# Performance work log

Measured on AMD Instinct MI355X. Metric: run time of the kernel, lower is better.

## Reference

```python
import jax, jax.numpy as jnp
import numpy as np

NUM_USERS = 100000
NUM_ITEMS = 100000
SEQ_LEN = 32
EMBED_DIM = 64
FC_DIM = 100
BATCH = 512
T = 3  # number of target items per example (train mode)


def setup_inputs() -> dict:
    key = jax.random.key(0)
    ks = jax.random.split(key, 12)
    seq_var = jax.random.randint(ks[0], (BATCH, SEQ_LEN), 0, NUM_ITEMS)
    user_var = jax.random.randint(ks[1], (BATCH, 1), 0, NUM_USERS)
    item_var = jax.random.randint(ks[2], (BATCH, T), 0, NUM_ITEMS)
    # Embedding tables, init normal(0, 1/dim) as in the torch module
    item_emb = jax.random.normal(ks[3], (NUM_ITEMS, EMBED_DIM)) * (1.0 / EMBED_DIM)
    user_emb = jax.random.normal(ks[4], (NUM_USERS, EMBED_DIM)) * (1.0 / EMBED_DIM)
    W2 = jax.random.normal(ks[5], (NUM_ITEMS, FC_DIM + EMBED_DIM)) * (1.0 / (FC_DIM + EMBED_DIM))
    b2 = jnp.zeros((NUM_ITEMS, 1))
    # nn.Linear default init: U(-1/sqrt(fan_in), 1/sqrt(fan_in))
    lim1 = 1.0 / np.sqrt(2 * EMBED_DIM)
    W1 = jax.random.uniform(ks[6], (FC_DIM, 2 * EMBED_DIM), minval=-lim1, maxval=lim1)
    b1 = jax.random.uniform(ks[7], (FC_DIM,), minval=-lim1, maxval=lim1)
    lim2 = 1.0 / np.sqrt(FC_DIM)
    Wf2 = jax.random.uniform(ks[8], (FC_DIM, FC_DIM), minval=-lim2, maxval=lim2)
    bf2 = jax.random.uniform(ks[9], (FC_DIM,), minval=-lim2, maxval=lim2)
    return dict(seq_var=seq_var, user_var=user_var, item_var=item_var,
                item_emb=item_emb, user_emb=user_emb, W2=W2, b2=b2,
                W1=W1, b1=b1, Wf2=Wf2, bf2=bf2)


def reference(seq_var, user_var, item_var, item_emb, user_emb, W2, b2, W1, b1, Wf2, bf2):
    # Dropout is identity in eval mode.
    d = item_emb.shape[1]
    embs = item_emb[seq_var]          # [B, L, d]
    uemb = user_emb[user_var]         # [B, 1, d]
    # fc1 on concat(item_i, item_j): split W1 columns so we never build the
    # [B, L, L, 2d] concat tensor; same math as Linear(cat([i, j])).
    Wa, Wb = W1[:, :d], W1[:, d:]     # [FC, d] each
    # all_embed[b, a, c] = cat(embs[b, c], embs[b, a])  (item_i varies with c)
    A = jnp.einsum('bld,fd->blf', embs, Wa)   # applied to item_i (index c)
    Bm = jnp.einsum('bld,fd->blf', embs, Wb)  # applied to item_j (index a)
    h = jax.nn.relu(A[:, None, :, :] + Bm[:, :, None, :] + b1)  # [B, L, L, FC]
    h = jax.nn.relu(jnp.einsum('bacf,gf->bacg', h, Wf2) + bf2)  # [B, L, L, FC]
    x = h.sum((1, 2))                               # [B, FC]
    x = jnp.concatenate([x, uemb[:, 0, :]], axis=1)  # [B, FC + d]
    w2 = W2[item_var]                                # [B, T, FC+d]
    bb = b2[item_var]                                # [B, T, 1]
    out = bb[..., 0] + jnp.einsum('btf,bf->bt', w2, x)  # baddbmm + squeeze -> [B, T]
    return out
```

## Files before the change

kernel.cpp:

```cpp
#include <hip/hip_runtime.h>

typedef float f32x4 __attribute__((ext_vector_type(4)));
typedef short short8 __attribute__((ext_vector_type(8)));
typedef _Float16 half8 __attribute__((ext_vector_type(8)));

#define SEQ_LEN 32
#define EMBED_DIM 64
#define FC_DIM 100
#define BATCH 512
#define AS 136
#define ES 72

union Frag {
  half8 h8;
  _Float16 h[8];
  short8 s;
  unsigned int u[4];
};

__global__ __launch_bounds__(256, 2) void cosrec_fused(
    const int* __restrict__ seq_var, const int* __restrict__ user_var,
    const int* __restrict__ item_var, const float* __restrict__ item_emb,
    const float* __restrict__ user_emb, const float* __restrict__ W2,
    const float* __restrict__ b2, const float* __restrict__ W1,
    const float* __restrict__ b1, const float* __restrict__ Wf2,
    const float* __restrict__ bf2, float* __restrict__ out)
{
  __shared__ __align__(16) _Float16 A_s[SEQ_LEN * AS];
  __shared__ __align__(16) _Float16 B_s[SEQ_LEN * AS];
  __shared__ float red_s[16 * 112];
  __shared__ float x_s[112];
  __shared__ __align__(16) _Float16 emb_s[SEQ_LEN * ES];

  const int b = blockIdx.x;
  const int t = threadIdx.x;
  const int w = t >> 6;
  const int l = t & 63;
  const int l15 = l & 15;
  const int q = l >> 4;
  const unsigned int biasbits = (q == 0) ? 0x00003C00u : 0u;

  {
    const int r = t >> 3;
    const int c0 = (t & 7) * 8;
    const int item = seq_var[b * SEQ_LEN + r];
    const float4 v0 = *(const float4*)(item_emb + item * EMBED_DIM + c0);
    const float4 v1 = *(const float4*)(item_emb + item * EMBED_DIM + c0 + 4);
    Frag e;
    e.h[0] = (_Float16)v0.x; e.h[1] = (_Float16)v0.y;
    e.h[2] = (_Float16)v0.z; e.h[3] = (_Float16)v0.w;
    e.h[4] = (_Float16)v1.x; e.h[5] = (_Float16)v1.y;
    e.h[6] = (_Float16)v1.z; e.h[7] = (_Float16)v1.w;
    *(short8*)(emb_s + r * ES + c0) = e.s;
  }
  for (int i = t; i < SEQ_LEN * 14; i += 256) {
    const int r = i / 14, d = (i % 14) * 2;
    *(unsigned int*)(A_s + r * AS + FC_DIM + d) = 0u;
    *(unsigned int*)(B_s + r * AS + FC_DIM + d) = 0u;
  }

  Frag wfrag[7][4];
  #pragma unroll
  for (int nt = 0; nt < 7; ++nt) {
    const int gg = nt * 16 + l15;
    const bool gok = (gg < FC_DIM);
    #pragma unroll
    for (int ks = 0; ks < 3; ++ks) {
      Frag f;
      if (gok) {
        const float4 u0 = *(const float4*)(Wf2 + gg * FC_DIM + ks * 32 + q * 8);
        const float4 u1 = *(const float4*)(Wf2 + gg * FC_DIM + ks * 32 + q * 8 + 4);
        f.h[0] = (_Float16)u0.x; f.h[1] = (_Float16)u0.y;
        f.h[2] = (_Float16)u0.z; f.h[3] = (_Float16)u0.w;
        f.h[4] = (_Float16)u1.x; f.h[5] = (_Float16)u1.y;
        f.h[6] = (_Float16)u1.z; f.h[7] = (_Float16)u1.w;
      } else {
        f.u[0] = 0u; f.u[1] = 0u; f.u[2] = 0u; f.u[3] = 0u;
      }
      wfrag[nt][ks] = f;
    }
    Frag f3;
    f3.u[0] = 0u; f3.u[1] = 0u; f3.u[2] = 0u; f3.u[3] = 0u;
    if (gok && q == 0) {
      const float4 u0 = *(const float4*)(Wf2 + gg * FC_DIM + 96);
      f3.h[0] = (_Float16)u0.x; f3.h[1] = (_Float16)u0.y;
      f3.h[2] = (_Float16)u0.z; f3.h[3] = (_Float16)u0.w;
      f3.h[4] = (_Float16)bf2[gg];
    }
    wfrag[nt][3] = f3;
  }
  __syncthreads();

  for (int nt = w; nt < 13; nt += 4) {
    const int o = nt * 16 + l15;
    int wr = 0, wc = 0;
    bool valid = true;
    if (o < FC_DIM)            { wr = o;          wc = 0;  }
    else if (o < 2 * FC_DIM)   { wr = o - FC_DIM; wc = 64; }
    else valid = false;
    Frag bfr[2];
    #pragma unroll
    for (int ks = 0; ks < 2; ++ks) {
      if (valid) {
        const float* p = W1 + wr * 128 + wc + ks * 32 + q * 8;
        const float4 u0 = *(const float4*)p;
        const float4 u1 = *(const float4*)(p + 4);
        bfr[ks].h[0] = (_Float16)u0.x; bfr[ks].h[1] = (_Float16)u0.y;
        bfr[ks].h[2] = (_Float16)u0.z; bfr[ks].h[3] = (_Float16)u0.w;
        bfr[ks].h[4] = (_Float16)u1.x; bfr[ks].h[5] = (_Float16)u1.y;
        bfr[ks].h[6] = (_Float16)u1.z; bfr[ks].h[7] = (_Float16)u1.w;
      } else {
        bfr[ks].u[0] = 0u; bfr[ks].u[1] = 0u; bfr[ks].u[2] = 0u; bfr[ks].u[3] = 0u;
      }
    }
    const float b1v = (o >= FC_DIM && o < 2 * FC_DIM) ? b1[o - FC_DIM] : 0.f;
    #pragma unroll
    for (int mt = 0; mt < 2; ++mt) {
      Frag afr[2];
      #pragma unroll
      for (int ks = 0; ks < 2; ++ks)
        afr[ks].s = *(const short8*)(emb_s + (mt * 16 + l15) * ES + ks * 32 + q * 8);
      f32x4 acc = {0.f, 0.f, 0.f, 0.f};
      #pragma unroll
      for (int ks = 0; ks < 2; ++ks)
        acc = __builtin_amdgcn_mfma_f32_16x16x32_f16(afr[ks].h8, bfr[ks].h8, acc, 0, 0, 0);
      const int row = mt * 16 + q * 4;
      if (o < FC_DIM) {
        #pragma unroll
        for (int r = 0; r < 4; ++r)
          A_s[(row + r) * AS + o] = (_Float16)acc[r];
      } else if (o < 2 * FC_DIM) {
        #pragma unroll
        for (int r = 0; r < 4; ++r)
          B_s[(row + r) * AS + (o - FC_DIM)] = (_Float16)(acc[r] + b1v);
      }
    }
  }
  __syncthreads();

  float colsum[7];
  #pragma unroll
  for (int nt = 0; nt < 7; ++nt) colsum[nt] = 0.f;
  const half8 hzero = {};

  for (int g = w; g < 8; g += 4) {
    const int c = (g & 1) * 16 + l15;
    const int a0 = (g >> 1) * 8;
    Frag areg[4];
    #pragma unroll
    for (int ks = 0; ks < 4; ++ks)
      areg[ks].s = *(const short8*)(A_s + c * AS + ks * 32 + q * 8);
    for (int ai = 0; ai < 8; ++ai) {
      const _Float16* bp = B_s + (a0 + ai) * AS;
      Frag hf[4];
      #pragma unroll
      for (int ks = 0; ks < 4; ++ks) {
        Frag br;
        br.s = *(const short8*)(bp + ks * 32 + q * 8);
        const half8 sum = areg[ks].h8 + br.h8;
        hf[ks].h8 = __builtin_elementwise_max(sum, hzero);
      }
      hf[3].u[2] |= biasbits;
      #pragma unroll
      for (int nt = 0; nt < 7; ++nt) {
        f32x4 acc = {0.f, 0.f, 0.f, 0.f};
        #pragma unroll
        for (int ks = 0; ks < 4; ++ks)
          acc = __builtin_amdgcn_mfma_f32_16x16x32_f16(hf[ks].h8, wfrag[nt][ks].h8, acc, 0, 0, 0);
        #pragma unroll
        for (int r = 0; r < 4; ++r)
          colsum[nt] += fmaxf(acc[r], 0.f);
      }
    }
  }

  #pragma unroll
  for (int nt = 0; nt < 7; ++nt)
    red_s[(w * 4 + q) * 112 + nt * 16 + l15] = colsum[nt];
  __syncthreads();
  if (t < 112) {
    float s = 0.f;
    #pragma unroll
    for (int r = 0; r < 16; ++r) s += red_s[r * 112 + t];
    x_s[t] = s;
  }
  __syncthreads();

  if (w < 3) {
    const int iv = item_var[b * 3 + w];
    const int uu = user_var[b];
    float partial = 0.f;
    for (int idx = l; idx < FC_DIM + EMBED_DIM; idx += 64) {
      const float xv = (idx < FC_DIM)
                           ? x_s[idx]
                           : user_emb[uu * EMBED_DIM + (idx - FC_DIM)];
      partial += W2[iv * (FC_DIM + EMBED_DIM) + idx] * xv;
    }
    #pragma unroll
    for (int off = 32; off > 0; off >>= 1)
      partial += __shfl_down(partial, off, 64);
    if (l == 0) out[b * 3 + w] = partial + b2[iv];
  }
}

extern "C" void kernel_launch(void* const* d_in, const int* in_sizes, int n_in,
                              void* d_out, int out_size, void* d_ws, size_t ws_size,
                              hipStream_t stream) {
  const int* seq = (const int*)d_in[0];
  const int* usr = (const int*)d_in[1];
  const int* itm = (const int*)d_in[2];
  const float* item_emb = (const float*)d_in[3];
  const float* user_emb = (const float*)d_in[4];
  const float* W2  = (const float*)d_in[5];
  const float* b2  = (const float*)d_in[6];
  const float* W1  = (const float*)d_in[7];
  const float* b1  = (const float*)d_in[8];
  const float* Wf2 = (const float*)d_in[9];
  const float* bf2 = (const float*)d_in[10];
  cosrec_fused<<<BATCH, 256, 0, stream>>>(seq, usr, itm, item_emb, user_emb,
                                          W2, b2, W1, b1, Wf2, bf2,
                                          (float*)d_out);
}
```

Measured before the change: 157.1 us.

## Prefetch W2/user/W1 operands early, double-buffer B rows, shuffle-based colsum reduction

Issues the W2 row, user embedding and b2 loads at kernel start so their latency overlaps the rest of the kernel. All W1 fragments are loaded into registers before the first barrier rather than inside the fc1 loop. In the pairwise loop, the next B_s row is prefetched into registers while the current row is computed. The column-sum reduction now uses wave shuffles followed by a single LDS pass, which removes one barrier and shrinks the reduction buffer, at the cost of higher register pressure.

```diff
diff --git a/kernel.cpp b/kernel.cpp
--- a/kernel.cpp
+++ b/kernel.cpp
@@ -28,8 +28,7 @@
 {
   __shared__ __align__(16) _Float16 A_s[SEQ_LEN * AS];
   __shared__ __align__(16) _Float16 B_s[SEQ_LEN * AS];
-  __shared__ float red_s[16 * 112];
-  __shared__ float x_s[112];
+  __shared__ float red_s[4 * 112];
   __shared__ __align__(16) _Float16 emb_s[SEQ_LEN * ES];
 
   const int b = blockIdx.x;
@@ -53,10 +52,17 @@
     e.h[6] = (_Float16)v1.z; e.h[7] = (_Float16)v1.w;
     *(short8*)(emb_s + r * ES + c0) = e.s;
   }
-  for (int i = t; i < SEQ_LEN * 14; i += 256) {
-    const int r = i / 14, d = (i % 14) * 2;
-    *(unsigned int*)(A_s + r * AS + FC_DIM + d) = 0u;
-    *(unsigned int*)(B_s + r * AS + FC_DIM + d) = 0u;
+
+  float w2a = 0.f, w2b = 0.f, w2c = 0.f, uev = 0.f, b2v = 0.f;
+  if (w < 3) {
+    const int iv = item_var[b * 3 + w];
+    const int uu = user_var[b];
+    const float* w2p = W2 + iv * (FC_DIM + EMBED_DIM);
+    w2a = w2p[l];
+    w2b = w2p[64 + l];
+    if (l < 36) w2c = w2p[128 + l];
+    uev = user_emb[uu * EMBED_DIM + (l >= 36 ? l - 36 : l + 28)];
+    b2v = b2[iv];
   }
 
   Frag wfrag[7][4];
@@ -89,50 +95,67 @@
     }
     wfrag[nt][3] = f3;
   }
+
+  Frag bfrh[4][2];
+  float b1h[4];
+  #pragma unroll
+  for (int i = 0; i < 4; ++i) {
+    const int nt = w + i * 4;
+    b1h[i] = 0.f;
+    bfrh[i][0].u[0] = 0u; bfrh[i][0].u[1] = 0u; bfrh[i][0].u[2] = 0u; bfrh[i][0].u[3] = 0u;
+    bfrh[i][1].u[0] = 0u; bfrh[i][1].u[1] = 0u; bfrh[i][1].u[2] = 0u; bfrh[i][1].u[3] = 0u;
+    if (nt < 13) {
+      const int o = nt * 16 + l15;
+      if (o < 2 * FC_DIM) {
+        const int wr = (o < FC_DIM) ? o : o - FC_DIM;
+        const int wc = (o < FC_DIM) ? 0 : 64;
+        #pragma unroll
+        for (int ks = 0; ks < 2; ++ks) {
+          const float* p = W1 + wr * 128 + wc + ks * 32 + q * 8;
+          const float4 u0 = *(const float4*)p;
+          const float4 u1 = *(const float4*)(p + 4);
+          bfrh[i][ks].h[0] = (_Float16)u0.x; bfrh[i][ks].h[1] = (_Float16)u0.y;
+          bfrh[i][ks].h[2] = (_Float16)u0.z; bfrh[i][ks].h[3] = (_Float16)u0.w;
+          bfrh[i][ks].h[4] = (_Float16)u1.x; bfrh[i][ks].h[5] = (_Float16)u1.y;
+          bfrh[i][ks].h[6] = (_Float16)u1.z; bfrh[i][ks].h[7] = (_Float16)u1.w;
+        }
+        if (o >= FC_DIM) b1h[i] = b1[o - FC_DIM];
+      }
+    }
+  }
+
+  for (int i = t; i < SEQ_LEN * 14; i += 256) {
+    const int r = i / 14, d = (i % 14) * 2;
+    *(unsigned int*)(A_s + r * AS + FC_DIM + d) = 0u;
+    *(unsigned int*)(B_s + r * AS + FC_DIM + d) = 0u;
+  }
   __syncthreads();
 
-  for (int nt = w; nt < 13; nt += 4) {
-    const int o = nt * 16 + l15;
-    int wr = 0, wc = 0;
-    bool valid = true;
-    if (o < FC_DIM)            { wr = o;          wc = 0;  }
-    else if (o < 2 * FC_DIM)   { wr = o - FC_DIM; wc = 64; }
-    else valid = false;
-    Frag bfr[2];
-    #pragma unroll
-    for (int ks = 0; ks < 2; ++ks) {
-      if (valid) {
-        const float* p = W1 + wr * 128 + wc + ks * 32 + q * 8;
-        const float4 u0 = *(const float4*)p;
-        const float4 u1 = *(const float4*)(p + 4);
-        bfr[ks].h[0] = (_Float16)u0.x; bfr[ks].h[1] = (_Float16)u0.y;
-        bfr[ks].h[2] = (_Float16)u0.z; bfr[ks].h[3] = (_Float16)u0.w;
-        bfr[ks].h[4] = (_Float16)u1.x; bfr[ks].h[5] = (_Float16)u1.y;
-        bfr[ks].h[6] = (_Float16)u1.z; bfr[ks].h[7] = (_Float16)u1.w;
-      } else {
-        bfr[ks].u[0] = 0u; bfr[ks].u[1] = 0u; bfr[ks].u[2] = 0u; bfr[ks].u[3] = 0u;
-      }
-    }
-    const float b1v = (o >= FC_DIM && o < 2 * FC_DIM) ? b1[o - FC_DIM] : 0.f;
-    #pragma unroll
-    for (int mt = 0; mt < 2; ++mt) {
-      Frag afr[2];
-      #pragma unroll
-      for (int ks = 0; ks < 2; ++ks)
-        afr[ks].s = *(const short8*)(emb_s + (mt * 16 + l15) * ES + ks * 32 + q * 8);
-      f32x4 acc = {0.f, 0.f, 0.f, 0.f};
-      #pragma unroll
-      for (int ks = 0; ks < 2; ++ks)
-        acc = __builtin_amdgcn_mfma_f32_16x16x32_f16(afr[ks].h8, bfr[ks].h8, acc, 0, 0, 0);
-      const int row = mt * 16 + q * 4;
-      if (o < FC_DIM) {
-        #pragma unroll
-        for (int r = 0; r < 4; ++r)
-          A_s[(row + r) * AS + o] = (_Float16)acc[r];
-      } else if (o < 2 * FC_DIM) {
-        #pragma unroll
-        for (int r = 0; r < 4; ++r)
-          B_s[(row + r) * AS + (o - FC_DIM)] = (_Float16)(acc[r] + b1v);
+  #pragma unroll
+  for (int i = 0; i < 4; ++i) {
+    const int nt = w + i * 4;
+    if (nt < 13) {
+      const int o = nt * 16 + l15;
+      #pragma unroll
+      for (int mt = 0; mt < 2; ++mt) {
+        Frag afr[2];
+        #pragma unroll
+        for (int ks = 0; ks < 2; ++ks)
+          afr[ks].s = *(const short8*)(emb_s + (mt * 16 + l15) * ES + ks * 32 + q * 8);
+        f32x4 acc = {0.f, 0.f, 0.f, 0.f};
+        #pragma unroll
+        for (int ks = 0; ks < 2; ++ks)
+          acc = __builtin_amdgcn_mfma_f32_16x16x32_f16(afr[ks].h8, bfrh[i][ks].h8, acc, 0, 0, 0);
+        const int row = mt * 16 + q * 4;
+        if (o < FC_DIM) {
+          #pragma unroll
+          for (int r = 0; r < 4; ++r)
+            A_s[(row + r) * AS + o] = (_Float16)acc[r];
+        } else if (o < 2 * FC_DIM) {
+          #pragma unroll
+          for (int r = 0; r < 4; ++r)
+            B_s[(row + r) * AS + (o - FC_DIM)] = (_Float16)(acc[r] + b1h[i]);
+        }
       }
     }
   }
@@ -150,14 +173,24 @@
     #pragma unroll
     for (int ks = 0; ks < 4; ++ks)
       areg[ks].s = *(const short8*)(A_s + c * AS + ks * 32 + q * 8);
+    Frag brn[4];
+    #pragma unroll
+    for (int ks = 0; ks < 4; ++ks)
+      brn[ks].s = *(const short8*)(B_s + a0 * AS + ks * 32 + q * 8);
     for (int ai = 0; ai < 8; ++ai) {
-      const _Float16* bp = B_s + (a0 + ai) * AS;
+      Frag br[4];
+      #pragma unroll
+      for (int ks = 0; ks < 4; ++ks) br[ks] = brn[ks];
+      if (ai < 7) {
+        const _Float16* bp = B_s + (a0 + ai + 1) * AS;
+        #pragma unroll
+        for (int ks = 0; ks < 4; ++ks)
+          brn[ks].s = *(const short8*)(bp + ks * 32 + q * 8);
+      }
       Frag hf[4];
       #pragma unroll
       for (int ks = 0; ks < 4; ++ks) {
-        Frag br;
-        br.s = *(const short8*)(bp + ks * 32 + q * 8);
-        const half8 sum = areg[ks].h8 + br.h8;
+        const half8 sum = areg[ks].h8 + br[ks].h8;
         hf[ks].h8 = __builtin_elementwise_max(sum, hzero);
       }
       hf[3].u[2] |= biasbits;
@@ -175,31 +208,30 @@
   }
 
   #pragma unroll
-  for (int nt = 0; nt < 7; ++nt)
-    red_s[(w * 4 + q) * 112 + nt * 16 + l15] = colsum[nt];
+  for (int nt = 0; nt < 7; ++nt) {
+    float v = colsum[nt];
+    v += __shfl_xor(v, 16, 64);
+    v += __shfl_xor(v, 32, 64);
+    if (l < 16) red_s[w * 112 + nt * 16 + l] = v;
+  }
   __syncthreads();
-  if (t < 112) {
-    float s = 0.f;
-    #pragma unroll
-    for (int r = 0; r < 16; ++r) s += red_s[r * 112 + t];
-    x_s[t] = s;
-  }
-  __syncthreads();
 
   if (w < 3) {
-    const int iv = item_var[b * 3 + w];
-    const int uu = user_var[b];
-    float partial = 0.f;
-    for (int idx = l; idx < FC_DIM + EMBED_DIM; idx += 64) {
-      const float xv = (idx < FC_DIM)
-                           ? x_s[idx]
-                           : user_emb[uu * EMBED_DIM + (idx - FC_DIM)];
-      partial += W2[iv * (FC_DIM + EMBED_DIM) + idx] * xv;
-    }
+    float xa = red_s[l] + red_s[112 + l] + red_s[224 + l] + red_s[336 + l];
+    float xb, xc;
+    if (l < 36) {
+      const int i2 = 64 + l;
+      xb = red_s[i2] + red_s[112 + i2] + red_s[224 + i2] + red_s[336 + i2];
+      xc = uev;
+    } else {
+      xb = uev;
+      xc = 0.f;
+    }
+    float partial = w2a * xa + w2b * xb + w2c * xc;
     #pragma unroll
     for (int off = 32; off > 0; off >>= 1)
       partial += __shfl_down(partial, off, 64);
-    if (l == 0) out[b * 3 + w] = partial + b2[iv];
+    if (l == 0) out[b * 3 + w] = partial + b2v;
   }
 }
 
```

After: 154.2 us. Within noise of the previous version (-1.8%).
